# Performance work log

Hardware: AMD Instinct MI355X
Metric: run time of the kernel (lower is better)

## Reference

```python
import jax, jax.numpy as jnp
import numpy as np


def setup_inputs() -> dict:
    key = jax.random.key(0)
    ks = jax.random.split(key, 7)
    B, S, D_IN, D_K, D_V = 4, 4096, 1024, 64, 64
    s = 1.0 / np.sqrt(D_IN)
    return {
        "query": jax.random.normal(ks[0], (B, S, D_IN), jnp.float32),
        "key": jax.random.normal(ks[1], (B, S, D_IN), jnp.float32),
        "value": jax.random.normal(ks[2], (B, S, D_IN), jnp.float32),
        "Wq": jax.random.normal(ks[3], (D_IN, D_K), jnp.float32) * s,
        "bq": jnp.zeros((D_K,), jnp.float32),
        "Wk": jax.random.normal(ks[4], (D_IN, D_K), jnp.float32) * s,
        "bk": jnp.zeros((D_K,), jnp.float32),
        "Wv": jax.random.normal(ks[5], (D_IN, D_V), jnp.float32) * s,
        "bv": jnp.zeros((D_V,), jnp.float32),
    }


def reference(query, key, value, Wq, bq, Wk, bk, Wv, bv):
    # q(query) is computed twice in the original but is identical; compute once.
    q = query @ Wq + bq            # [B,S,dk]
    k = key @ Wk + bk              # [B,S,dk]
    v = value @ Wv + bv            # [B,S,dv]
    scale = jnp.asarray(q.shape[-1] ** 0.5, q.dtype)
    scores = jnp.einsum("bqd,bkd->bqk", q, k) / scale  # [B,S,S]
    probs = jax.nn.softmax(scores, axis=-1)
    return jnp.einsum("bqk,bkd->bqd", probs, v)        # [B,S,dv]
```

## Files before the change

kernel.cpp:

```cpp
#include <hip/hip_runtime.h>
#include <cmath>

constexpr int B_  = 4;
constexpr int S_  = 4096;
constexpr int DIN = 1024;
constexpr int DH  = 64;

typedef short bf16x8 __attribute__((ext_vector_type(8)));
typedef float f32x4  __attribute__((ext_vector_type(4)));

#define GPTR(p) (const __attribute__((address_space(1))) unsigned int*)(p)
#define LPTR(p) (__attribute__((address_space(3))) unsigned int*)(p)

__device__ __forceinline__ ushort f2bf(float x) {
    unsigned int u = __float_as_uint(x);
    return (ushort)((u + 0x7FFFu + ((u >> 16) & 1u)) >> 16);
}

__device__ __forceinline__ bf16x8 cvt8(float4 a, float4 b) {
    union { bf16x8 v; ushort u[8]; } r;
    r.u[0] = f2bf(a.x); r.u[1] = f2bf(a.y); r.u[2] = f2bf(a.z); r.u[3] = f2bf(a.w);
    r.u[4] = f2bf(b.x); r.u[5] = f2bf(b.y); r.u[6] = f2bf(b.z); r.u[7] = f2bf(b.w);
    return r.v;
}

#define QSCALE 0.18033688011112042f

__global__ __launch_bounds__(256) void setup_w(
    const float* __restrict__ Wq, const float* __restrict__ Wk,
    const float* __restrict__ Wv, ushort* __restrict__ Wt_g)
{
    const int y = blockIdx.y;
    const float* W = (y == 0) ? Wq : (y == 1) ? Wk : Wv;
    const int g   = blockIdx.x * 256 + threadIdx.x;
    const int p   = g & 7;
    const int n   = (g >> 3) & 63;
    const int win = g >> 9;
    const int k0  = win * 64 + p * 8;
    union { uint4 q; ushort u[8]; } r;
    #pragma unroll
    for (int i = 0; i < 8; ++i) r.u[i] = f2bf(W[(size_t)(k0 + i) * DH + n]);
    *(uint4*)(Wt_g + ((size_t)y << 16) + (size_t)(((win * 64 + n) * 8 + p) * 8)) = r.q;
}

__global__ __launch_bounds__(256, 3) void proj_kernel(
    const float* __restrict__ Xq, const float* __restrict__ Xk, const float* __restrict__ Xv,
    const float* __restrict__ bq, const float* __restrict__ bk, const float* __restrict__ bv,
    const ushort* __restrict__ Wt_g,
    ushort* __restrict__ Qb, ushort* __restrict__ Kb, ushort* __restrict__ Vt)
{
    const int y = blockIdx.y;
    const float *X, *bias;
    if (y == 0)      { X = Xq; bias = bq; }
    else if (y == 1) { X = Xk; bias = bk; }
    else             { X = Xv; bias = bv; }

    __shared__ ushort Vx[64 * 72];

    const int tid  = threadIdx.x;
    const int w    = tid >> 6;
    const int lane = tid & 63;
    const int m    = lane & 15;
    const int quad = lane >> 4;
    const int row0 = blockIdx.x * 64;

    const size_t  xrow  = (size_t)(row0 + w * 16 + m) * DIN;
    const ushort* wbase = Wt_g + ((size_t)y << 16);

    float bias_v[4];
    #pragma unroll
    for (int nt = 0; nt < 4; ++nt) bias_v[nt] = bias[nt * 16 + m];

    f32x4 acc[4] = {};

    float4 xcur[4], xnxt[4];
    bf16x8 wcur[8], wnxt[8];

    {
        const float* px = X + xrow + quad * 8;
        xcur[0] = *(const float4*)(px);      xcur[1] = *(const float4*)(px + 4);
        xcur[2] = *(const float4*)(px + 32); xcur[3] = *(const float4*)(px + 36);
        #pragma unroll
        for (int ks = 0; ks < 2; ++ks)
            #pragma unroll
            for (int nt = 0; nt < 4; ++nt)
                wcur[ks * 4 + nt] = *(const bf16x8*)(wbase
                    + (size_t)(((nt * 16 + m) * 8 + ks * 4 + quad) * 8));
    }

    for (int it = 0; it < 16; ++it) {
        if (it < 15) {
            const float* px = X + xrow + (it + 1) * 64 + quad * 8;
            xnxt[0] = *(const float4*)(px);      xnxt[1] = *(const float4*)(px + 4);
            xnxt[2] = *(const float4*)(px + 32); xnxt[3] = *(const float4*)(px + 36);
            #pragma unroll
            for (int ks = 0; ks < 2; ++ks)
                #pragma unroll
                for (int nt = 0; nt < 4; ++nt)
                    wnxt[ks * 4 + nt] = *(const bf16x8*)(wbase
                        + (size_t)((((it + 1) * 64 + nt * 16 + m) * 8 + ks * 4 + quad) * 8));
        }
        #pragma unroll
        for (int ks = 0; ks < 2; ++ks) {
            const bf16x8 a = cvt8(xcur[ks * 2], xcur[ks * 2 + 1]);
            #pragma unroll
            for (int nt = 0; nt < 4; ++nt)
                acc[nt] = __builtin_amdgcn_mfma_f32_16x16x32_bf16(
                    a, wcur[ks * 4 + nt], acc[nt], 0, 0, 0);
        }
        #pragma unroll
        for (int i = 0; i < 4; ++i) xcur[i] = xnxt[i];
        #pragma unroll
        for (int i = 0; i < 8; ++i) wcur[i] = wnxt[i];
    }

    if (y < 2) {
        ushort* Out = (y == 0) ? Qb : Kb;
        const float sc = (y == 0) ? QSCALE : 1.0f;
        #pragma unroll
        for (int nt = 0; nt < 4; ++nt)
            #pragma unroll
            for (int j = 0; j < 4; ++j) {
                const int row = row0 + w * 16 + quad * 4 + j;
                Out[(size_t)row * DH + nt * 16 + m] = f2bf((acc[nt][j] + bias_v[nt]) * sc);
            }
    } else {
        #pragma unroll
        for (int nt = 0; nt < 4; ++nt)
            #pragma unroll
            for (int j = 0; j < 4; ++j) {
                const int d = nt * 16 + m;
                const int s = w * 16 + quad * 4 + j;
                Vx[d * 72 + (((s >> 3) ^ (d & 7)) * 8) + (s & 7)] = f2bf(acc[nt][j] + bias_v[nt]);
            }
        __syncthreads();
        const int batch = row0 >> 12;
        const int s0    = row0 & 4095;
        for (int i = tid; i < 512; i += 256) {
            const int d = i >> 3, c = i & 7;
            const uint4 v = *(const uint4*)&Vx[d * 72 + ((c ^ (d & 7)) * 8)];
            *(uint4*)(Vt + ((size_t)batch * 64 + d) * S_ + s0 + c * 8) = v;
        }
    }
}

__global__ __launch_bounds__(256, 3) void attn_kernel(
    const ushort* __restrict__ Qb, const ushort* __restrict__ Kb,
    const ushort* __restrict__ Vt, float* __restrict__ Opart, float* __restrict__ Lpart)
{
    __shared__ ushort Ks[2][4096];
    __shared__ ushort Vs[2][4096];
    __shared__ ushort Pt[64 * 72];

    const int tid  = threadIdx.x;
    const int w    = tid >> 6;
    const int lane = tid & 63;
    const int m    = lane & 15;
    const int quad = lane >> 4;
    const int b    = blockIdx.z, jc = blockIdx.y, qt = blockIdx.x;
    const int q0   = qt * 64;

    bf16x8 qf[2];
    #pragma unroll
    for (int ks = 0; ks < 2; ++ks)
        qf[ks] = *(const bf16x8*)(Qb + (size_t)(b * S_ + q0 + w * 16 + m) * 64
                                     + ks * 32 + quad * 8);

    f32x4 acc_o[4] = {};
    float Lp[4] = {};

    const ushort* kbase = Kb + (size_t)b * S_ * 64;
    const ushort* vbase = Vt + (size_t)b * 64 * S_;

    const int slot0 = w * 128 + lane;
    const int j0 = slot0 >> 3, c0 = slot0 & 7;
    const int j1 = (slot0 + 64) >> 3, c1 = (slot0 + 64) & 7;

    #define ISSUE_DMA(IT, NB)                                                          \
        do {                                                                           \
            const int _jt = jc * 16 + (IT);                                            \
            __builtin_amdgcn_global_load_lds(                                          \
                GPTR(kbase + (size_t)(_jt * 64 + j0) * 64 + ((c0 ^ (j0 & 7)) * 8)),    \
                LPTR(&Ks[NB][(w * 128) * 8]), 16, 0, 0);                               \
            __builtin_amdgcn_global_load_lds(                                          \
                GPTR(kbase + (size_t)(_jt * 64 + j1) * 64 + ((c1 ^ (j1 & 7)) * 8)),    \
                LPTR(&Ks[NB][(w * 128 + 64) * 8]), 16, 0, 0);                          \
            __builtin_amdgcn_global_load_lds(                                          \
                GPTR(vbase + (size_t)j0 * S_ + _jt * 64 + ((c0 ^ (j0 & 7)) * 8)),      \
                LPTR(&Vs[NB][(w * 128) * 8]), 16, 0, 0);                               \
            __builtin_amdgcn_global_load_lds(                                          \
                GPTR(vbase + (size_t)j1 * S_ + _jt * 64 + ((c1 ^ (j1 & 7)) * 8)),      \
                LPTR(&Vs[NB][(w * 128 + 64) * 8]), 16, 0, 0);                          \
        } while (0)

    ISSUE_DMA(0, 0);

    for (int it = 0; it < 16; ++it) {
        __syncthreads();
        if (it < 15) ISSUE_DMA(it + 1, (it + 1) & 1);
        const int cb = it & 1;

        f32x4 acc_s[4] = {};
        #pragma unroll
        for (int ks = 0; ks < 2; ++ks)
            #pragma unroll
            for (int jt4 = 0; jt4 < 4; ++jt4) {
                const int j = jt4 * 16 + m;
                const bf16x8 kf = *(const bf16x8*)&Ks[cb][j * 64 + (((ks * 4 + quad) ^ (j & 7)) * 8)];
                acc_s[jt4] = __builtin_amdgcn_mfma_f32_16x16x32_bf16(
                    qf[ks], kf, acc_s[jt4], 0, 0, 0);
            }

        #pragma unroll
        for (int jt4 = 0; jt4 < 4; ++jt4)
            #pragma unroll
            for (int r = 0; r < 4; ++r) {
                const float e = exp2f(acc_s[jt4][r]);
                Lp[r] += e;
                Pt[(w * 16 + quad * 4 + r) * 72 + jt4 * 16 + m] = f2bf(e);
            }

        #pragma unroll
        for (int jc2 = 0; jc2 < 2; ++jc2) {
            const bf16x8 pf = *(const bf16x8*)&Pt[(w * 16 + m) * 72 + jc2 * 32 + quad * 8];
            #pragma unroll
            for (int dt = 0; dt < 4; ++dt) {
                const int d = dt * 16 + m;
                const bf16x8 vf = *(const bf16x8*)&Vs[cb][d * 64 + (((jc2 * 4 + quad) ^ (d & 7)) * 8)];
                acc_o[dt] = __builtin_amdgcn_mfma_f32_16x16x32_bf16(pf, vf, acc_o[dt], 0, 0, 0);
            }
        }
    }
    #undef ISSUE_DMA

    #pragma unroll
    for (int r = 0; r < 4; ++r) {
        float s = Lp[r];
        #pragma unroll
        for (int off = 1; off < 16; off <<= 1)
            s += __shfl_xor(s, off, 64);
        Lp[r] = s;
    }

    const size_t bj = (size_t)(b * 4 + jc);
    float* Ob = Opart + (bj << 18);
    #pragma unroll
    for (int dt = 0; dt < 4; ++dt)
        #pragma unroll
        for (int r = 0; r < 4; ++r) {
            const int row = q0 + w * 16 + quad * 4 + r;
            Ob[(size_t)row * 64 + dt * 16 + m] = acc_o[dt][r];
        }
    if (m == 0) {
        #pragma unroll
        for (int r = 0; r < 4; ++r)
            Lpart[bj * 4096 + q0 + w * 16 + quad * 4 + r] = Lp[r];
    }
}

__global__ __launch_bounds__(256) void reduce_kernel(
    const float* __restrict__ Opart, const float* __restrict__ Lpart, float* __restrict__ out)
{
    const int g    = blockIdx.x * 256 + threadIdx.x;
    const int base = g << 2;
    const int b    = base >> 18;
    const int rem  = base & 0x3FFFF;
    const int q    = rem >> 6;
    float4 o = make_float4(0.f, 0.f, 0.f, 0.f);
    float  l = 0.f;
    #pragma unroll
    for (int jcc = 0; jcc < 4; ++jcc) {
        const float4 p = *(const float4*)(Opart + (((size_t)(b * 4 + jcc)) << 18) + rem);
        o.x += p.x; o.y += p.y; o.z += p.z; o.w += p.w;
        l += Lpart[(size_t)(b * 4 + jcc) * 4096 + q];
    }
    const float inv = 1.0f / l;
    o.x *= inv; o.y *= inv; o.z *= inv; o.w *= inv;
    *(float4*)(out + base) = o;
}

extern "C" void kernel_launch(void* const* d_in, const int* in_sizes, int n_in,
                              void* d_out, int out_size, void* d_ws, size_t ws_size,
                              hipStream_t stream)
{
    const float* query = (const float*)d_in[0];
    const float* key_  = (const float*)d_in[1];
    const float* value = (const float*)d_in[2];
    const float* Wq    = (const float*)d_in[3];
    const float* bq    = (const float*)d_in[4];
    const float* Wk    = (const float*)d_in[5];
    const float* bk    = (const float*)d_in[6];
    const float* Wv    = (const float*)d_in[7];
    const float* bv    = (const float*)d_in[8];
    float* out = (float*)d_out;

    char* ws = (char*)d_ws;
    ushort* Qb    = (ushort*)(ws);
    ushort* Kb    = (ushort*)(ws + (2  << 20));
    ushort* Vt    = (ushort*)(ws + (4  << 20));
    float*  Opart = (float*) (ws + (6  << 20));
    float*  Lpart = (float*) (ws + (22 << 20));
    ushort* Wt_g  = (ushort*)(ws + (6  << 20));

    setup_w<<<dim3(32, 3), 256, 0, stream>>>(Wq, Wk, Wv, Wt_g);
    proj_kernel<<<dim3(256, 3), 256, 0, stream>>>(
        query, key_, value, bq, bk, bv, Wt_g, Qb, Kb, Vt);
    attn_kernel<<<dim3(64, 4, 4), 256, 0, stream>>>(Qb, Kb, Vt, Opart, Lpart);
    reduce_kernel<<<dim3(1024), 256, 0, stream>>>(Opart, Lpart, out);
}
```

Before: 284.6 us.

## Stage projection X tiles in LDS via async global_load_lds with swizzle

```diff
diff --git a/kernel.cpp b/kernel.cpp
--- a/kernel.cpp
+++ b/kernel.cpp
@@ -26,21 +26,32 @@
 
 #define QSCALE 0.18033688011112042f
 
+__device__ __forceinline__ int xswz(int c, int r) {
+    return (c & 8) | ((c & 7) ^ (r & 7));
+}
+
 __global__ __launch_bounds__(256) void setup_w(
     const float* __restrict__ Wq, const float* __restrict__ Wk,
     const float* __restrict__ Wv, ushort* __restrict__ Wt_g)
 {
-    const int y = blockIdx.y;
+    __shared__ ushort Ws[64 * 72];
+    const int y = blockIdx.y, win = blockIdx.x, tid = threadIdx.x;
     const float* W = (y == 0) ? Wq : (y == 1) ? Wk : Wv;
-    const int g   = blockIdx.x * 256 + threadIdx.x;
-    const int p   = g & 7;
-    const int n   = (g >> 3) & 63;
-    const int win = g >> 9;
-    const int k0  = win * 64 + p * 8;
-    union { uint4 q; ushort u[8]; } r;
-    #pragma unroll
-    for (int i = 0; i < 8; ++i) r.u[i] = f2bf(W[(size_t)(k0 + i) * DH + n]);
-    *(uint4*)(Wt_g + ((size_t)y << 16) + (size_t)(((win * 64 + n) * 8 + p) * 8)) = r.q;
+
+    for (int i = tid; i < 1024; i += 256) {
+        const int k = i >> 4, n4 = (i & 15) << 2;
+        const float4 f = *(const float4*)(W + (size_t)(win * 64 + k) * DH + n4);
+        Ws[(n4 + 0) * 72 + k] = f2bf(f.x);
+        Ws[(n4 + 1) * 72 + k] = f2bf(f.y);
+        Ws[(n4 + 2) * 72 + k] = f2bf(f.z);
+        Ws[(n4 + 3) * 72 + k] = f2bf(f.w);
+    }
+    __syncthreads();
+    for (int i = tid; i < 512; i += 256) {
+        const int p = i >> 6, n = i & 63;
+        const uint4 v = *(const uint4*)&Ws[n * 72 + p * 8];
+        *(uint4*)(Wt_g + ((size_t)y << 16) + (size_t)(((win * 8 + p) * 64 + n) * 8)) = v;
+    }
 }
 
 __global__ __launch_bounds__(256, 3) void proj_kernel(
@@ -55,7 +66,7 @@
     else if (y == 1) { X = Xk; bias = bk; }
     else             { X = Xv; bias = bv; }
 
-    __shared__ ushort Vx[64 * 72];
+    __shared__ float Xs[2][4096];
 
     const int tid  = threadIdx.x;
     const int w    = tid >> 6;
@@ -64,53 +75,66 @@
     const int quad = lane >> 4;
     const int row0 = blockIdx.x * 64;
 
-    const size_t  xrow  = (size_t)(row0 + w * 16 + m) * DIN;
     const ushort* wbase = Wt_g + ((size_t)y << 16);
 
     float bias_v[4];
     #pragma unroll
     for (int nt = 0; nt < 4; ++nt) bias_v[nt] = bias[nt * 16 + m];
 
+    int dma_row[4], dma_koff[4];
+    #pragma unroll
+    for (int i = 0; i < 4; ++i) {
+        const int g = (w * 4 + i) * 64 + lane;
+        dma_row[i]  = g >> 4;
+        dma_koff[i] = xswz(g & 15, g >> 4) * 4;
+    }
+
+    #define ISSUE_X(IT, NB)                                                         \
+        do {                                                                        \
+            _Pragma("unroll")                                                       \
+            for (int i = 0; i < 4; ++i)                                             \
+                __builtin_amdgcn_global_load_lds(                                   \
+                    GPTR(X + (size_t)(row0 + dma_row[i]) * DIN + (IT) * 64          \
+                         + dma_koff[i]),                                            \
+                    LPTR(&Xs[NB][(w * 4 + i) * 256]), 16, 0, 0);                    \
+        } while (0)
+
     f32x4 acc[4] = {};
-
-    float4 xcur[4], xnxt[4];
     bf16x8 wcur[8], wnxt[8];
 
-    {
-        const float* px = X + xrow + quad * 8;
-        xcur[0] = *(const float4*)(px);      xcur[1] = *(const float4*)(px + 4);
-        xcur[2] = *(const float4*)(px + 32); xcur[3] = *(const float4*)(px + 36);
-        #pragma unroll
-        for (int ks = 0; ks < 2; ++ks)
-            #pragma unroll
-            for (int nt = 0; nt < 4; ++nt)
-                wcur[ks * 4 + nt] = *(const bf16x8*)(wbase
-                    + (size_t)(((nt * 16 + m) * 8 + ks * 4 + quad) * 8));
-    }
-
+    ISSUE_X(0, 0);
+    #pragma unroll
+    for (int ks = 0; ks < 2; ++ks)
+        #pragma unroll
+        for (int nt = 0; nt < 4; ++nt)
+            wcur[ks * 4 + nt] = *(const bf16x8*)(wbase
+                + (size_t)(((ks * 4 + quad) * 64 + nt * 16 + m) * 8));
+
+    const int r = w * 16 + m;
     for (int it = 0; it < 16; ++it) {
+        __syncthreads();
         if (it < 15) {
-            const float* px = X + xrow + (it + 1) * 64 + quad * 8;
-            xnxt[0] = *(const float4*)(px);      xnxt[1] = *(const float4*)(px + 4);
-            xnxt[2] = *(const float4*)(px + 32); xnxt[3] = *(const float4*)(px + 36);
+            ISSUE_X(it + 1, (it + 1) & 1);
             #pragma unroll
             for (int ks = 0; ks < 2; ++ks)
                 #pragma unroll
                 for (int nt = 0; nt < 4; ++nt)
                     wnxt[ks * 4 + nt] = *(const bf16x8*)(wbase
-                        + (size_t)((((it + 1) * 64 + nt * 16 + m) * 8 + ks * 4 + quad) * 8));
-        }
+                        + (size_t)((((it + 1) * 8 + ks * 4 + quad) * 64 + nt * 16 + m) * 8));
+        }
+        const float* buf = Xs[it & 1];
         #pragma unroll
         for (int ks = 0; ks < 2; ++ks) {
-            const bf16x8 a = cvt8(xcur[ks * 2], xcur[ks * 2 + 1]);
+            const int c0 = ks * 8 + quad * 2;
+            const float4 xa = *(const float4*)&buf[r * 64 + xswz(c0, m) * 4];
+            const float4 xb = *(const float4*)&buf[r * 64 + xswz(c0 + 1, m) * 4];
+            const bf16x8 a = cvt8(xa, xb);
             #pragma unroll
             for (int nt = 0; nt < 4; ++nt)
                 acc[nt] = __builtin_amdgcn_mfma_f32_16x16x32_bf16(
                     a, wcur[ks * 4 + nt], acc[nt], 0, 0, 0);
         }
         #pragma unroll
-        for (int i = 0; i < 4; ++i) xcur[i] = xnxt[i];
-        #pragma unroll
         for (int i = 0; i < 8; ++i) wcur[i] = wnxt[i];
     }
 
@@ -125,6 +149,8 @@
                 Out[(size_t)row * DH + nt * 16 + m] = f2bf((acc[nt][j] + bias_v[nt]) * sc);
             }
     } else {
+        __syncthreads();
+        ushort* Vx = (ushort*)&Xs[0][0];
         #pragma unroll
         for (int nt = 0; nt < 4; ++nt)
             #pragma unroll
@@ -142,6 +168,7 @@
             *(uint4*)(Vt + ((size_t)batch * 64 + d) * S_ + s0 + c * 8) = v;
         }
     }
+    #undef ISSUE_X
 }
 
 __global__ __launch_bounds__(256, 3) void attn_kernel(
@@ -302,7 +329,7 @@
     float*  Lpart = (float*) (ws + (22 << 20));
     ushort* Wt_g  = (ushort*)(ws + (6  << 20));
 
-    setup_w<<<dim3(32, 3), 256, 0, stream>>>(Wq, Wk, Wv, Wt_g);
+    setup_w<<<dim3(16, 3), 256, 0, stream>>>(Wq, Wk, Wv, Wt_g);
     proj_kernel<<<dim3(256, 3), 256, 0, stream>>>(
         query, key_, value, bq, bk, bv, Wt_g, Qb, Kb, Vt);
     attn_kernel<<<dim3(64, 4, 4), 256, 0, stream>>>(Qb, Kb, Vt, Opart, Lpart);
```

Result: faster. 273.6 us (-3.9%).
